# Kernel optimization log

Hardware: AMD Instinct MI355X
Metric: run time of the kernel (lower is better)

## Reference

```python
import jax, jax.numpy as jnp
import numpy as np

B, C, H, W = 32, 512, 32, 32
HID, MEM = 256, 256


def setup_inputs() -> dict:
    key = jax.random.key(0)
    k1, k2, k3, k4, k5, k6 = jax.random.split(key, 6)
    x = jax.random.normal(k1, (B, C, H, W), dtype=jnp.float32)
    h = jax.random.normal(k2, (B, MEM), dtype=jnp.float32)
    # conv1: 1x1 conv, no bias -> weight [HID, C]
    W_conv1 = jax.random.normal(k3, (HID, C), dtype=jnp.float32) / np.sqrt(C)
    # linear1: memory_dim -> hidden_dim, with bias
    W_lin = jax.random.normal(k4, (HID, MEM), dtype=jnp.float32) / np.sqrt(MEM)
    b_lin = jax.random.normal(k5, (HID,), dtype=jnp.float32) * 0.01
    # attention_conv: 1x1 conv hidden->1, no bias -> weight [HID]
    W_attn = jax.random.normal(k6, (HID,), dtype=jnp.float32) / np.sqrt(HID)
    return {"x": x, "h": h, "W_conv1": W_conv1, "W_lin": W_lin,
            "b_lin": b_lin, "W_attn": W_attn}


def reference(x, h, W_conv1, W_lin, b_lin, W_attn):
    # x: [B,C,H,W], h: [B,MEM]
    x2 = x.reshape(x.shape[0], x.shape[1], -1)            # [B,C,HW]
    x3 = jnp.einsum('bchw,kc->bkhw', x, W_conv1)          # 1x1 conv -> [B,HID,H,W]
    h3 = (h @ W_lin.T + b_lin)[:, :, None, None]          # [B,HID,1,1] broadcast over H,W
    a1 = jnp.tanh(x3 + h3)                                # [B,HID,H,W]
    a2 = jnp.einsum('bkhw,k->bhw', a1, W_attn).reshape(x.shape[0], -1)  # [B,HW]
    a3 = jax.nn.softmax(a2, axis=1)                       # [B,HW]
    context = jnp.einsum('bcs,bs->bc', x2, a3)            # [B,C]
    return (a3, context)
```

## Files before the change

### kernel.cpp

```cpp
#include <hip/hip_runtime.h>
#include <hip/hip_bf16.h>
#include <cmath>


typedef __bf16 bf16;
typedef __attribute__((ext_vector_type(8))) __bf16 bf16x8;
typedef __attribute__((ext_vector_type(4))) float f32x4;

__global__ __launch_bounds__(256) void prep_kernel(const float* __restrict__ h,
                                                   const float* __restrict__ Wlin,
                                                   const float* __restrict__ blin,
                                                   const float* __restrict__ Wc,
                                                   float* __restrict__ h3,
                                                   bf16* __restrict__ Whi,
                                                   bf16* __restrict__ Wlo) {
    const int tid = threadIdx.x;
    if (blockIdx.x < 32) {
        const int b = blockIdx.x;
        __shared__ float hs[256];
        hs[tid] = h[b * 256 + tid];
        __syncthreads();
        const float4* wr = (const float4*)(Wlin + (size_t)tid * 256);
        float acc = blin[tid];
        #pragma unroll 8
        for (int q = 0; q < 64; ++q) {
            float4 w = wr[q];
            float4 hv = *(const float4*)&hs[q * 4];
            acc = fmaf(w.x, hv.x, fmaf(w.y, hv.y, fmaf(w.z, hv.z, fmaf(w.w, hv.w, acc))));
        }
        h3[b * 256 + tid] = acc;
    } else {
        const int e0 = (blockIdx.x - 32) * 2048 + tid * 8;
        float4 v0 = *(const float4*)(Wc + e0);
        float4 v1 = *(const float4*)(Wc + e0 + 4);
        float vs[8] = {v0.x, v0.y, v0.z, v0.w, v1.x, v1.y, v1.z, v1.w};
        bf16x8 vh, vl;
        #pragma unroll
        for (int j = 0; j < 8; ++j) {
            bf16 hi = (bf16)vs[j];
            float r = vs[j] - (float)hi;
            vh[j] = hi;
            vl[j] = (bf16)r;
        }
        *(bf16x8*)&Whi[e0] = vh;
        *(bf16x8*)&Wlo[e0] = vl;
    }
}

__global__ __launch_bounds__(256, 3) void fused_mfma(const float* __restrict__ x,
                                                     const bf16* __restrict__ Whi,
                                                     const bf16* __restrict__ Wlo,
                                                     const float* __restrict__ h3,
                                                     const float* __restrict__ Wattn,
                                                     float* __restrict__ a2) {
    __shared__ bf16 Ahi[128 * 64];
    __shared__ bf16 Alo[128 * 64];
    __shared__ bf16 Bhi[64 * 64];
    __shared__ bf16 Blo[64 * 64];
    __shared__ float red2[4 * 64];

    const int tid = threadIdx.x;
    const int bid = blockIdx.x;
    const int wk = (bid & 7) * 128 + (bid >> 3);
    const int b  = wk >> 5;
    const int st = (wk >> 1) & 15;
    const int mb = wk & 1;
    const int s0 = st * 64;
    const int r0 = mb * 128;

    const int w  = tid >> 6;
    const int l  = tid & 63;
    const int g  = l >> 4;
    const int lr = l & 15;

    const float* xb = x + ((size_t)b << 19);

    f32x4 acc[2][4];
    #pragma unroll
    for (int mf = 0; mf < 2; ++mf)
        #pragma unroll
        for (int nf = 0; nf < 4; ++nf)
            acc[mf][nf] = (f32x4){0.f, 0.f, 0.f, 0.f};

    const int arow_ = tid >> 3;
    const int acol  = (tid & 7) * 8;
    const int bs    = (tid >> 3) * 2;
    const int bc_   = (tid & 7) * 2;

    #pragma unroll 1
    for (int c0 = 0; c0 < 512; c0 += 64) {
        bf16x8 wva[4], wvl[4];
        #pragma unroll
        for (int jj = 0; jj < 4; ++jj) {
            int row = arow_ + 32 * jj;
            size_t off = (size_t)(r0 + row) * 512 + c0 + acol;
            wva[jj] = *(const bf16x8*)(Whi + off);
            wvl[jj] = *(const bf16x8*)(Wlo + off);
        }
        float2 xv0[4], xv1[4];
        #pragma unroll
        for (int jj = 0; jj < 4; ++jj) {
            int cc = bc_ + 16 * jj;
            xv0[jj] = *(const float2*)(xb + (size_t)(c0 + cc) * 1024 + s0 + bs);
            xv1[jj] = *(const float2*)(xb + (size_t)(c0 + cc + 1) * 1024 + s0 + bs);
        }
        __syncthreads();
        #pragma unroll
        for (int jj = 0; jj < 4; ++jj) {
            int row = arow_ + 32 * jj;
            int idx = row * 64 + (acol ^ (8 * (row & 7)));
            *(bf16x8*)&Ahi[idx] = wva[jj];
            *(bf16x8*)&Alo[idx] = wvl[jj];
        }
        #pragma unroll
        for (int jj = 0; jj < 4; ++jj) {
            int cc = bc_ + 16 * jj;
            bf16 h00 = (bf16)xv0[jj].x, h10 = (bf16)xv1[jj].x;
            bf16 h01 = (bf16)xv0[jj].y, h11 = (bf16)xv1[jj].y;
            bf16 l00 = (bf16)(xv0[jj].x - (float)h00), l10 = (bf16)(xv1[jj].x - (float)h10);
            bf16 l01 = (bf16)(xv0[jj].y - (float)h01), l11 = (bf16)(xv1[jj].y - (float)h11);
            int i0 = bs * 64 + (cc ^ (8 * (bs & 7)));
            int i1 = (bs + 1) * 64 + (cc ^ (8 * ((bs + 1) & 7)));
            Bhi[i0] = h00; Bhi[i0 + 1] = h10;
            Blo[i0] = l00; Blo[i0 + 1] = l10;
            Bhi[i1] = h01; Bhi[i1 + 1] = h11;
            Blo[i1] = l01; Blo[i1 + 1] = l11;
        }
        __syncthreads();
        #pragma unroll
        for (int kk = 0; kk < 2; ++kk) {
            bf16x8 ah[2], al[2], bh[4], bl[4];
            #pragma unroll
            for (int mf = 0; mf < 2; ++mf) {
                int row = w * 32 + mf * 16 + lr;
                int idx = row * 64 + ((kk * 32 + 8 * g) ^ (8 * (row & 7)));
                ah[mf] = *(const bf16x8*)&Ahi[idx];
                al[mf] = *(const bf16x8*)&Alo[idx];
            }
            #pragma unroll
            for (int nf = 0; nf < 4; ++nf) {
                int srow = nf * 16 + lr;
                int idx = srow * 64 + ((kk * 32 + 8 * g) ^ (8 * (srow & 7)));
                bh[nf] = *(const bf16x8*)&Bhi[idx];
                bl[nf] = *(const bf16x8*)&Blo[idx];
            }
            #pragma unroll
            for (int mf = 0; mf < 2; ++mf)
                #pragma unroll
                for (int nf = 0; nf < 4; ++nf) {
                    acc[mf][nf] = __builtin_amdgcn_mfma_f32_16x16x32_bf16(ah[mf], bh[nf], acc[mf][nf], 0, 0, 0);
                    acc[mf][nf] = __builtin_amdgcn_mfma_f32_16x16x32_bf16(ah[mf], bl[nf], acc[mf][nf], 0, 0, 0);
                    acc[mf][nf] = __builtin_amdgcn_mfma_f32_16x16x32_bf16(al[mf], bh[nf], acc[mf][nf], 0, 0, 0);
                }
        }
    }

    const float* h3b = h3 + b * 256;
    float part[4] = {0.f, 0.f, 0.f, 0.f};
    #pragma unroll
    for (int mf = 0; mf < 2; ++mf) {
        #pragma unroll
        for (int i = 0; i < 4; ++i) {
            int kch = r0 + w * 32 + mf * 16 + g * 4 + i;
            float hv = h3b[kch];
            float wt = Wattn[kch];
            #pragma unroll
            for (int nf = 0; nf < 4; ++nf)
                part[nf] += wt * tanhf(acc[mf][nf][i] + hv);
        }
    }
    #pragma unroll
    for (int nf = 0; nf < 4; ++nf) {
        part[nf] += __shfl_xor(part[nf], 16, 64);
        part[nf] += __shfl_xor(part[nf], 32, 64);
    }
    if (l < 16) {
        #pragma unroll
        for (int nf = 0; nf < 4; ++nf) red2[w * 64 + nf * 16 + l] = part[nf];
    }
    __syncthreads();
    if (tid < 64) {
        float tot = red2[tid] + red2[64 + tid] + red2[128 + tid] + red2[192 + tid];
        atomicAdd(&a2[(size_t)b * 1024 + s0 + tid], tot);
    }
}

__global__ __launch_bounds__(256) void softmax_context(const float* __restrict__ x,
                                                       const float* __restrict__ a2,
                                                       float* __restrict__ a3,
                                                       float* __restrict__ ctx) {
    __shared__ float sm[1024];
    __shared__ float red[8];
    const int tid = threadIdx.x;
    const int b = blockIdx.y, ct = blockIdx.x;
    const int wave = tid >> 6, lane = tid & 63;

    float4 v = ((const float4*)(a2 + (size_t)b * 1024))[tid];
    float m = fmaxf(fmaxf(v.x, v.y), fmaxf(v.z, v.w));
    #pragma unroll
    for (int off = 32; off >= 1; off >>= 1) m = fmaxf(m, __shfl_xor(m, off, 64));
    if (lane == 0) red[wave] = m;
    __syncthreads();
    m = fmaxf(fmaxf(red[0], red[1]), fmaxf(red[2], red[3]));
    float e0 = expf(v.x - m), e1 = expf(v.y - m), e2 = expf(v.z - m), e3 = expf(v.w - m);
    float s = e0 + e1 + e2 + e3;
    #pragma unroll
    for (int off = 32; off >= 1; off >>= 1) s += __shfl_xor(s, off, 64);
    if (lane == 0) red[4 + wave] = s;
    __syncthreads();
    s = red[4] + red[5] + red[6] + red[7];
    float inv = 1.f / s;
    float4 o = {e0 * inv, e1 * inv, e2 * inv, e3 * inv};
    ((float4*)sm)[tid] = o;
    if (ct == 0) ((float4*)(a3 + (size_t)b * 1024))[tid] = o;
    __syncthreads();

    const float* xb = x + ((size_t)b << 19);
    #pragma unroll
    for (int r = 0; r < 8; ++r) {
        int c = ct * 32 + wave * 8 + r;
        const float4* row = (const float4*)(xb + (size_t)c * 1024);
        float sum = 0.f;
        #pragma unroll
        for (int it = 0; it < 4; ++it) {
            int idx = it * 64 + lane;
            float4 xv = row[idx];
            float4 av = *(const float4*)&sm[idx * 4];
            sum = fmaf(xv.x, av.x, fmaf(xv.y, av.y, fmaf(xv.z, av.z, fmaf(xv.w, av.w, sum))));
        }
        #pragma unroll
        for (int off = 32; off >= 1; off >>= 1) sum += __shfl_xor(sum, off, 64);
        if (lane == 0) ctx[(size_t)b * 512 + c] = sum;
    }
}

extern "C" void kernel_launch(void* const* d_in, const int* in_sizes, int n_in,
                              void* d_out, int out_size, void* d_ws, size_t ws_size,
                              hipStream_t stream) {
    const float* x     = (const float*)d_in[0];
    const float* h     = (const float*)d_in[1];
    const float* Wc    = (const float*)d_in[2];
    const float* Wlin  = (const float*)d_in[3];
    const float* blin  = (const float*)d_in[4];
    const float* Wattn = (const float*)d_in[5];

    float* out = (float*)d_out;
    float* a3  = out;
    float* ctx = out + 32 * 1024;

    char* ws = (char*)d_ws;
    float* h3 = (float*)ws;
    float* a2 = (float*)(ws + 32768);
    bf16* Whi = (bf16*)(ws + 32768 + 131072);
    bf16* Wlo = (bf16*)(ws + 32768 + 131072 + 262144);

    hipMemsetAsync(a2, 0, 32 * 1024 * sizeof(float), stream);
    hipLaunchKernelGGL(prep_kernel, dim3(96), dim3(256), 0, stream, h, Wlin, blin, Wc, h3, Whi, Wlo);
    hipLaunchKernelGGL(fused_mfma, dim3(1024), dim3(256), 0, stream, x, Whi, Wlo, h3, Wattn, a2);
    hipLaunchKernelGGL(softmax_context, dim3(16, 32), dim3(256), 0, stream, x, a2, a3, ctx);
}
```

Before: 162.7 us.

## Restructure fused MFMA kernel with full-hidden tiles, async LDS x staging, 32x32 MFMA

Each block of the fused kernel now computes all 256 hidden channels for a 64-position tile instead of half. The x tensor is therefore read once rather than twice, and the atomicAdd with its memset goes away. Weight fragments are loaded straight from global memory into registers. x tiles are double-buffered into LDS with global_load_lds, then split into hi/lo bf16 fragments, and the math uses 32x32x16 MFMA. Occupancy drops to two blocks per CU. The softmax/context kernel now uses twice as many blocks, each handling fewer channels.

```diff
diff --git a/kernel.cpp b/kernel.cpp
--- a/kernel.cpp
+++ b/kernel.cpp
@@ -5,7 +5,7 @@
 
 typedef __bf16 bf16;
 typedef __attribute__((ext_vector_type(8))) __bf16 bf16x8;
-typedef __attribute__((ext_vector_type(4))) float f32x4;
+typedef __attribute__((ext_vector_type(16))) float f32x16;
 
 __global__ __launch_bounds__(256) void prep_kernel(const float* __restrict__ h,
                                                    const float* __restrict__ Wlin,
@@ -47,141 +47,136 @@
     }
 }
 
-__global__ __launch_bounds__(256, 3) void fused_mfma(const float* __restrict__ x,
+__global__ __launch_bounds__(256, 2) void fused_mfma(const float* __restrict__ x,
                                                      const bf16* __restrict__ Whi,
                                                      const bf16* __restrict__ Wlo,
                                                      const float* __restrict__ h3,
                                                      const float* __restrict__ Wattn,
                                                      float* __restrict__ a2) {
-    __shared__ bf16 Ahi[128 * 64];
-    __shared__ bf16 Alo[128 * 64];
-    __shared__ bf16 Bhi[64 * 64];
-    __shared__ bf16 Blo[64 * 64];
+    __shared__ float xbuf[2][64 * 64];
+    __shared__ bf16x8 fragB[16 * 64];
     __shared__ float red2[4 * 64];
 
     const int tid = threadIdx.x;
     const int bid = blockIdx.x;
-    const int wk = (bid & 7) * 128 + (bid >> 3);
-    const int b  = wk >> 5;
-    const int st = (wk >> 1) & 15;
-    const int mb = wk & 1;
-    const int s0 = st * 64;
-    const int r0 = mb * 128;
+    const int wk = (bid & 7) * 64 + (bid >> 3);
+    const int b  = wk >> 4;
+    const int s0 = (wk & 15) * 64;
 
     const int w  = tid >> 6;
     const int l  = tid & 63;
-    const int g  = l >> 4;
-    const int lr = l & 15;
-
-    const float* xb = x + ((size_t)b << 19);
-
-    f32x4 acc[2][4];
+    const int h  = l >> 5;
+    const int lr = l & 31;
+
+    const float* xb = x + ((size_t)b << 19) + s0;
+
+    const bf16* aphi[2];
+    const bf16* aplo[2];
+    #pragma unroll
+    for (int mf = 0; mf < 2; ++mf) {
+        const size_t kr = (size_t)(64 * w + 32 * mf + lr) * 512 + 8 * h;
+        aphi[mf] = Whi + kr;
+        aplo[mf] = Wlo + kr;
+    }
+
+    f32x16 acc[2][2];
     #pragma unroll
     for (int mf = 0; mf < 2; ++mf)
         #pragma unroll
-        for (int nf = 0; nf < 4; ++nf)
-            acc[mf][nf] = (f32x4){0.f, 0.f, 0.f, 0.f};
-
-    const int arow_ = tid >> 3;
-    const int acol  = (tid & 7) * 8;
-    const int bs    = (tid >> 3) * 2;
-    const int bc_   = (tid & 7) * 2;
+        for (int nf = 0; nf < 2; ++nf)
+            #pragma unroll
+            for (int r = 0; r < 16; ++r) acc[mf][nf][r] = 0.f;
+
+    auto stage = [&](int tt, int nb) {
+        #pragma unroll
+        for (int q = 0; q < 4; ++q) {
+            const float* g = xb + (size_t)(tt * 64 + 16 * q + 4 * w + (l >> 4)) * 1024
+                                + 4 * (l & 15);
+            __builtin_amdgcn_global_load_lds(
+                (const __attribute__((address_space(1))) void*)g,
+                (__attribute__((address_space(3))) void*)((char*)&xbuf[nb][0] + q * 4096 + w * 1024),
+                16, 0, 0);
+        }
+    };
+
+    stage(0, 0);
 
     #pragma unroll 1
-    for (int c0 = 0; c0 < 512; c0 += 64) {
-        bf16x8 wva[4], wvl[4];
-        #pragma unroll
-        for (int jj = 0; jj < 4; ++jj) {
-            int row = arow_ + 32 * jj;
-            size_t off = (size_t)(r0 + row) * 512 + c0 + acol;
-            wva[jj] = *(const bf16x8*)(Whi + off);
-            wvl[jj] = *(const bf16x8*)(Wlo + off);
-        }
-        float2 xv0[4], xv1[4];
-        #pragma unroll
-        for (int jj = 0; jj < 4; ++jj) {
-            int cc = bc_ + 16 * jj;
-            xv0[jj] = *(const float2*)(xb + (size_t)(c0 + cc) * 1024 + s0 + bs);
-            xv1[jj] = *(const float2*)(xb + (size_t)(c0 + cc + 1) * 1024 + s0 + bs);
-        }
+    for (int t = 0; t < 8; ++t) {
+        const int cur = t & 1;
+        const int c0 = t * 64;
         __syncthreads();
-        #pragma unroll
-        for (int jj = 0; jj < 4; ++jj) {
-            int row = arow_ + 32 * jj;
-            int idx = row * 64 + (acol ^ (8 * (row & 7)));
-            *(bf16x8*)&Ahi[idx] = wva[jj];
-            *(bf16x8*)&Alo[idx] = wvl[jj];
-        }
-        #pragma unroll
-        for (int jj = 0; jj < 4; ++jj) {
-            int cc = bc_ + 16 * jj;
-            bf16 h00 = (bf16)xv0[jj].x, h10 = (bf16)xv1[jj].x;
-            bf16 h01 = (bf16)xv0[jj].y, h11 = (bf16)xv1[jj].y;
-            bf16 l00 = (bf16)(xv0[jj].x - (float)h00), l10 = (bf16)(xv1[jj].x - (float)h10);
-            bf16 l01 = (bf16)(xv0[jj].y - (float)h01), l11 = (bf16)(xv1[jj].y - (float)h11);
-            int i0 = bs * 64 + (cc ^ (8 * (bs & 7)));
-            int i1 = (bs + 1) * 64 + (cc ^ (8 * ((bs + 1) & 7)));
-            Bhi[i0] = h00; Bhi[i0 + 1] = h10;
-            Blo[i0] = l00; Blo[i0 + 1] = l10;
-            Bhi[i1] = h01; Bhi[i1 + 1] = h11;
-            Blo[i1] = l01; Blo[i1 + 1] = l11;
+
+        bf16x8 ah[2][4], al[2][4];
+        #pragma unroll
+        for (int mf = 0; mf < 2; ++mf)
+            #pragma unroll
+            for (int kk = 0; kk < 4; ++kk) {
+                ah[mf][kk] = *(const bf16x8*)(aphi[mf] + c0 + 16 * kk);
+                al[mf][kk] = *(const bf16x8*)(aplo[mf] + c0 + 16 * kk);
+            }
+
+        #pragma unroll
+        for (int nf = 0; nf < 2; ++nf) {
+            const int base = (16 * w + 8 * h) * 64 + 32 * nf + lr;
+            float f[8];
+            #pragma unroll
+            for (int j = 0; j < 8; ++j) f[j] = xbuf[cur][base + j * 64];
+            bf16x8 vh, vl;
+            #pragma unroll
+            for (int j = 0; j < 8; ++j) {
+                bf16 hh = (bf16)f[j];
+                vh[j] = hh;
+                vl[j] = (bf16)(f[j] - (float)hh);
+            }
+            fragB[(w * 4 + nf * 2 + 0) * 64 + l] = vh;
+            fragB[(w * 4 + nf * 2 + 1) * 64 + l] = vl;
         }
         __syncthreads();
-        #pragma unroll
-        for (int kk = 0; kk < 2; ++kk) {
-            bf16x8 ah[2], al[2], bh[4], bl[4];
+
+        if (t < 7) stage(t + 1, cur ^ 1);
+
+        #pragma unroll
+        for (int kk = 0; kk < 4; ++kk) {
+            bf16x8 bh0 = fragB[(kk * 4 + 0) * 64 + l];
+            bf16x8 bl0 = fragB[(kk * 4 + 1) * 64 + l];
+            bf16x8 bh1 = fragB[(kk * 4 + 2) * 64 + l];
+            bf16x8 bl1 = fragB[(kk * 4 + 3) * 64 + l];
             #pragma unroll
             for (int mf = 0; mf < 2; ++mf) {
-                int row = w * 32 + mf * 16 + lr;
-                int idx = row * 64 + ((kk * 32 + 8 * g) ^ (8 * (row & 7)));
-                ah[mf] = *(const bf16x8*)&Ahi[idx];
-                al[mf] = *(const bf16x8*)&Alo[idx];
+                acc[mf][0] = __builtin_amdgcn_mfma_f32_32x32x16_bf16(ah[mf][kk], bh0, acc[mf][0], 0, 0, 0);
+                acc[mf][0] = __builtin_amdgcn_mfma_f32_32x32x16_bf16(ah[mf][kk], bl0, acc[mf][0], 0, 0, 0);
+                acc[mf][0] = __builtin_amdgcn_mfma_f32_32x32x16_bf16(al[mf][kk], bh0, acc[mf][0], 0, 0, 0);
+                acc[mf][1] = __builtin_amdgcn_mfma_f32_32x32x16_bf16(ah[mf][kk], bh1, acc[mf][1], 0, 0, 0);
+                acc[mf][1] = __builtin_amdgcn_mfma_f32_32x32x16_bf16(ah[mf][kk], bl1, acc[mf][1], 0, 0, 0);
+                acc[mf][1] = __builtin_amdgcn_mfma_f32_32x32x16_bf16(al[mf][kk], bh1, acc[mf][1], 0, 0, 0);
             }
-            #pragma unroll
-            for (int nf = 0; nf < 4; ++nf) {
-                int srow = nf * 16 + lr;
-                int idx = srow * 64 + ((kk * 32 + 8 * g) ^ (8 * (srow & 7)));
-                bh[nf] = *(const bf16x8*)&Bhi[idx];
-                bl[nf] = *(const bf16x8*)&Blo[idx];
-            }
-            #pragma unroll
-            for (int mf = 0; mf < 2; ++mf)
-                #pragma unroll
-                for (int nf = 0; nf < 4; ++nf) {
-                    acc[mf][nf] = __builtin_amdgcn_mfma_f32_16x16x32_bf16(ah[mf], bh[nf], acc[mf][nf], 0, 0, 0);
-                    acc[mf][nf] = __builtin_amdgcn_mfma_f32_16x16x32_bf16(ah[mf], bl[nf], acc[mf][nf], 0, 0, 0);
-                    acc[mf][nf] = __builtin_amdgcn_mfma_f32_16x16x32_bf16(al[mf], bh[nf], acc[mf][nf], 0, 0, 0);
-                }
         }
     }
 
     const float* h3b = h3 + b * 256;
-    float part[4] = {0.f, 0.f, 0.f, 0.f};
+    float part[2] = {0.f, 0.f};
     #pragma unroll
     for (int mf = 0; mf < 2; ++mf) {
         #pragma unroll
-        for (int i = 0; i < 4; ++i) {
-            int kch = r0 + w * 32 + mf * 16 + g * 4 + i;
-            float hv = h3b[kch];
-            float wt = Wattn[kch];
-            #pragma unroll
-            for (int nf = 0; nf < 4; ++nf)
-                part[nf] += wt * tanhf(acc[mf][nf][i] + hv);
-        }
-    }
-    #pragma unroll
-    for (int nf = 0; nf < 4; ++nf) {
-        part[nf] += __shfl_xor(part[nf], 16, 64);
-        part[nf] += __shfl_xor(part[nf], 32, 64);
-    }
-    if (l < 16) {
-        #pragma unroll
-        for (int nf = 0; nf < 4; ++nf) red2[w * 64 + nf * 16 + l] = part[nf];
+        for (int r = 0; r < 16; ++r) {
+            const int k = 64 * w + 32 * mf + (r & 3) + 8 * (r >> 2) + 4 * h;
+            const float hv = h3b[k];
+            const float wt = Wattn[k];
+            part[0] += wt * tanhf(acc[mf][0][r] + hv);
+            part[1] += wt * tanhf(acc[mf][1][r] + hv);
+        }
+    }
+    part[0] += __shfl_xor(part[0], 32, 64);
+    part[1] += __shfl_xor(part[1], 32, 64);
+    if (l < 32) {
+        red2[w * 64 + lr]      = part[0];
+        red2[w * 64 + 32 + lr] = part[1];
     }
     __syncthreads();
     if (tid < 64) {
-        float tot = red2[tid] + red2[64 + tid] + red2[128 + tid] + red2[192 + tid];
-        atomicAdd(&a2[(size_t)b * 1024 + s0 + tid], tot);
+        a2[(size_t)b * 1024 + s0 + tid] =
+            red2[tid] + red2[64 + tid] + red2[128 + tid] + red2[192 + tid];
     }
 }
 
@@ -217,8 +212,8 @@
 
     const float* xb = x + ((size_t)b << 19);
     #pragma unroll
-    for (int r = 0; r < 8; ++r) {
-        int c = ct * 32 + wave * 8 + r;
+    for (int r = 0; r < 4; ++r) {
+        int c = ct * 16 + wave * 4 + r;
         const float4* row = (const float4*)(xb + (size_t)c * 1024);
         float sum = 0.f;
         #pragma unroll
@@ -254,8 +249,7 @@
     bf16* Whi = (bf16*)(ws + 32768 + 131072);
     bf16* Wlo = (bf16*)(ws + 32768 + 131072 + 262144);
 
-    hipMemsetAsync(a2, 0, 32 * 1024 * sizeof(float), stream);
     hipLaunchKernelGGL(prep_kernel, dim3(96), dim3(256), 0, stream, h, Wlin, blin, Wc, h3, Whi, Wlo);
-    hipLaunchKernelGGL(fused_mfma, dim3(1024), dim3(256), 0, stream, x, Whi, Wlo, h3, Wattn, a2);
-    hipLaunchKernelGGL(softmax_context, dim3(16, 32), dim3(256), 0, stream, x, a2, a3, ctx);
-}
+    hipLaunchKernelGGL(fused_mfma, dim3(512), dim3(256), 0, stream, x, Whi, Wlo, h3, Wattn, a2);
+    hipLaunchKernelGGL(softmax_context, dim3(32, 32), dim3(256), 0, stream, x, a2, a3, ctx);
+}
```

After: 157.8 us. 3.1% less time.
